# Kernel tuning notes

Measured on AMD Instinct MI355X. Metric: run time of the kernel, lower is better.

The kernel has to match this reference:

```python
import jax, jax.numpy as jnp
import numpy as np

BN_EPS = 1e-5

def relu6(v):
    return jnp.clip(v, 0.0, 6.0)

def setup_inputs() -> dict:
    key = jax.random.key(0)
    ks = jax.random.split(key, 7)
    C, R = 512, 128  # in_channels, reduced_channels = C // 4
    B, H, W = 8, 128, 128
    x = jax.random.normal(ks[0], (B, C, H, W), dtype=jnp.float32)
    # 1x1 convs stored as [out_ch, in_ch] matrices (kernel is 1x1, no bias)
    w_guide = jax.random.normal(ks[1], (R, C), dtype=jnp.float32) * (1.0 / np.sqrt(C))
    w_fuse = jax.random.normal(ks[2], (C, R), dtype=jnp.float32) * (1.0 / np.sqrt(R))
    bn_gamma = jax.random.normal(ks[3], (C,), dtype=jnp.float32) * 0.1 + 1.0
    bn_beta = jax.random.normal(ks[4], (C,), dtype=jnp.float32) * 0.1
    bn_mean = jax.random.normal(ks[5], (C,), dtype=jnp.float32) * 0.1
    bn_var = jax.random.uniform(ks[6], (C,), dtype=jnp.float32, minval=0.5, maxval=1.5)
    return {"x": x, "w_guide": w_guide, "w_fuse": w_fuse,
            "bn_gamma": bn_gamma, "bn_beta": bn_beta,
            "bn_mean": bn_mean, "bn_var": bn_var}

def reference(x, w_guide, w_fuse, bn_gamma, bn_beta, bn_mean, bn_var):
    # y = AdaptiveAvgPool2d(1)(x): [B, C]
    y = jnp.mean(x, axis=(2, 3))
    # conv_guide: 1x1 conv (no bias) + ReLU6 on the 1x1 map -> [B, R]
    y = relu6(jnp.einsum('rc,bc->br', w_guide, y))
    # Nearest upsample of a 1x1 map then pointwise conv+BN+ReLU6 commutes:
    # compute conv_fuse once per (b, channel), then broadcast over H, W.
    y = jnp.einsum('cr,br->bc', w_fuse, y)  # 1x1 conv, no bias -> [B, C]
    inv_std = jax.lax.rsqrt(bn_var + BN_EPS)
    y = relu6((y - bn_mean) * inv_std * bn_gamma + bn_beta)
    # residual add with nearest-broadcast of the constant spatial map
    return x + y[:, :, None, None]
```

## Files before the change

kernel.cpp:

```cpp
#include <hip/hip_runtime.h>

#define C_CH  512
#define R_CH  128
#define BATCH 8
#define HW    16384
#define HW4   (HW / 4)
#define NPLANE (BATCH * C_CH)
#define PPB   4
#define NBLK  (NPLANE / PPB)

typedef float floatx4 __attribute__((ext_vector_type(4)));

__device__ __forceinline__ float relu6f(float v) {
    return fminf(fmaxf(v, 0.0f), 6.0f);
}

__global__ __launch_bounds__(256) void mean_kernel(const float4* __restrict__ x,
                                                   float* __restrict__ meanv) {
    const int plane = blockIdx.x;
    const float4* px = x + (size_t)plane * HW4;
    float s = 0.0f;
#pragma unroll
    for (int it = 0; it < HW4 / 256; ++it) {
        float4 v = px[threadIdx.x + it * 256];
        s += (v.x + v.y) + (v.z + v.w);
    }
    __shared__ float red[256];
    red[threadIdx.x] = s;
    __syncthreads();
    for (int off = 128; off > 0; off >>= 1) {
        if (threadIdx.x < off) red[threadIdx.x] += red[threadIdx.x + off];
        __syncthreads();
    }
    if (threadIdx.x == 0) meanv[plane] = red[0] * (1.0f / (float)HW);
}

__global__ __launch_bounds__(256) void fused_kernel(
    const float4* __restrict__ x,
    const float* __restrict__ meanv,
    const float* __restrict__ wg,
    const float* __restrict__ wf,
    const float* __restrict__ gamma,
    const float* __restrict__ beta,
    const float* __restrict__ mu,
    const float* __restrict__ var,
    float4* __restrict__ out) {
    const int g = (NBLK - 1) - (int)blockIdx.x;
    const int plane0 = g * PPB;
    const int b = plane0 >> 9;
    const int c0 = plane0 & (C_CH - 1);

    __shared__ float m[C_CH];
    __shared__ float part[256];
    __shared__ float t[R_CH];
    __shared__ float yv[PPB];

    const int tid = threadIdx.x;
    for (int c = tid; c < C_CH; c += 256) m[c] = meanv[b * C_CH + c];
    __syncthreads();

    {
        const int r = tid & (R_CH - 1);
        const int half = tid >> 7;
        const float4* w4 = (const float4*)(wg + (size_t)r * C_CH) + half * (C_CH / 8);
        const float* mh = m + half * (C_CH / 2);
        float a0 = 0.f, a1 = 0.f;
#pragma unroll 8
        for (int i = 0; i < C_CH / 8; ++i) {
            float4 v = w4[i];
            const int c = i * 4;
            a0 += v.x * mh[c + 0] + v.y * mh[c + 1];
            a1 += v.z * mh[c + 2] + v.w * mh[c + 3];
        }
        part[tid] = a0 + a1;
    }
    __syncthreads();
    if (tid < R_CH) t[tid] = relu6f(part[tid] + part[tid + R_CH]);
    __syncthreads();

    if (tid < PPB) {
        const int c = c0 + tid;
        const float4* w4 = (const float4*)(wf + (size_t)c * R_CH);
        float a0 = 0.f, a1 = 0.f;
#pragma unroll
        for (int i = 0; i < R_CH / 4; ++i) {
            float4 v = w4[i];
            const int r = i * 4;
            a0 += v.x * t[r + 0] + v.y * t[r + 1];
            a1 += v.z * t[r + 2] + v.w * t[r + 3];
        }
        const float s = a0 + a1;
        const float inv_std = 1.0f / sqrtf(var[c] + 1e-5f);
        yv[tid] = relu6f((s - mu[c]) * inv_std * gamma[c] + beta[c]);
    }
    __syncthreads();

#pragma unroll
    for (int p = 0; p < PPB; ++p) {
        const float a = yv[p];
        const float4* px = x + (size_t)(plane0 + p) * HW4;
        floatx4* po = reinterpret_cast<floatx4*>(out + (size_t)(plane0 + p) * HW4);
#pragma unroll
        for (int it = 0; it < HW4 / 256; ++it) {
            const int i = tid + it * 256;
            float4 v = px[i];
            floatx4 w;
            w.x = v.x + a; w.y = v.y + a; w.z = v.z + a; w.w = v.w + a;
            __builtin_nontemporal_store(w, po + i);
        }
    }
}

extern "C" void kernel_launch(void* const* d_in, const int* in_sizes, int n_in,
                              void* d_out, int out_size, void* d_ws, size_t ws_size,
                              hipStream_t stream) {
    const float4* x4  = (const float4*)d_in[0];
    const float* wg   = (const float*)d_in[1];
    const float* wf   = (const float*)d_in[2];
    const float* gamma = (const float*)d_in[3];
    const float* beta  = (const float*)d_in[4];
    const float* mu    = (const float*)d_in[5];
    const float* var   = (const float*)d_in[6];

    float* meanv = (float*)d_ws;
    float4* out  = (float4*)d_out;

    mean_kernel<<<NPLANE, 256, 0, stream>>>(x4, meanv);
    fused_kernel<<<NBLK, 256, 0, stream>>>(x4, meanv, wg, wf, gamma, beta,
                                           mu, var, out);
}
```

Before: 509.1 us.

## Chunk mean and add passes so second read of x hits cache

Splits the two full passes over x into four chunks of 1024 planes (two batches each). The launches are interleaved: mean for chunk k+1 runs before add for chunk k. The aim is for the second read of each chunk to come from the large last-level cache instead of HBM. It also cuts planes per add block from 4 to 2 and uses nontemporal loads in the add pass. The cost is more kernel launches with smaller grids, plus some risk that the interleaved working set does not stay resident in cache.

Result: slower. 546.1 us (+7.3%).

```diff
diff --git a/kernel.cpp b/kernel.cpp
--- a/kernel.cpp
+++ b/kernel.cpp
@@ -6,8 +6,11 @@
 #define HW    16384
 #define HW4   (HW / 4)
 #define NPLANE (BATCH * C_CH)
-#define PPB   4
-#define NBLK  (NPLANE / PPB)
+#define TPB   256
+#define PPB   2
+#define CHUNK_PLANES 1024
+#define MEAN_BLOCKS  CHUNK_PLANES
+#define ADD_BLOCKS   (CHUNK_PLANES / PPB)
 
 typedef float floatx4 __attribute__((ext_vector_type(4)));
 
@@ -15,28 +18,29 @@
     return fminf(fmaxf(v, 0.0f), 6.0f);
 }
 
-__global__ __launch_bounds__(256) void mean_kernel(const float4* __restrict__ x,
-                                                   float* __restrict__ meanv) {
-    const int plane = blockIdx.x;
+__global__ __launch_bounds__(TPB) void mean_kernel(const float4* __restrict__ x,
+                                                   float* __restrict__ meanv,
+                                                   int plane_base) {
+    const int plane = plane_base + blockIdx.x;
     const float4* px = x + (size_t)plane * HW4;
     float s = 0.0f;
 #pragma unroll
-    for (int it = 0; it < HW4 / 256; ++it) {
-        float4 v = px[threadIdx.x + it * 256];
+    for (int it = 0; it < HW4 / TPB; ++it) {
+        float4 v = px[threadIdx.x + it * TPB];
         s += (v.x + v.y) + (v.z + v.w);
     }
-    __shared__ float red[256];
+    __shared__ float red[TPB];
     red[threadIdx.x] = s;
     __syncthreads();
-    for (int off = 128; off > 0; off >>= 1) {
+    for (int off = TPB / 2; off > 0; off >>= 1) {
         if (threadIdx.x < off) red[threadIdx.x] += red[threadIdx.x + off];
         __syncthreads();
     }
     if (threadIdx.x == 0) meanv[plane] = red[0] * (1.0f / (float)HW);
 }
 
-__global__ __launch_bounds__(256) void fused_kernel(
-    const float4* __restrict__ x,
+__global__ __launch_bounds__(TPB) void add_kernel(
+    const floatx4* __restrict__ x,
     const float* __restrict__ meanv,
     const float* __restrict__ wg,
     const float* __restrict__ wf,
@@ -44,19 +48,19 @@
     const float* __restrict__ beta,
     const float* __restrict__ mu,
     const float* __restrict__ var,
-    float4* __restrict__ out) {
-    const int g = (NBLK - 1) - (int)blockIdx.x;
-    const int plane0 = g * PPB;
-    const int b = plane0 >> 9;
+    floatx4* __restrict__ out,
+    int plane_base) {
+    const int plane0 = plane_base + (int)blockIdx.x * PPB;
+    const int b  = plane0 >> 9;
     const int c0 = plane0 & (C_CH - 1);
+    const int tid = threadIdx.x;
 
     __shared__ float m[C_CH];
-    __shared__ float part[256];
+    __shared__ float part[TPB];
     __shared__ float t[R_CH];
-    __shared__ float yv[PPB];
+    __shared__ float ys[PPB];
 
-    const int tid = threadIdx.x;
-    for (int c = tid; c < C_CH; c += 256) m[c] = meanv[b * C_CH + c];
+    for (int c = tid; c < C_CH; c += TPB) m[c] = meanv[b * C_CH + c];
     __syncthreads();
 
     {
@@ -91,22 +95,21 @@
         }
         const float s = a0 + a1;
         const float inv_std = 1.0f / sqrtf(var[c] + 1e-5f);
-        yv[tid] = relu6f((s - mu[c]) * inv_std * gamma[c] + beta[c]);
+        ys[tid] = relu6f((s - mu[c]) * inv_std * gamma[c] + beta[c]);
     }
     __syncthreads();
 
 #pragma unroll
     for (int p = 0; p < PPB; ++p) {
-        const float a = yv[p];
-        const float4* px = x + (size_t)(plane0 + p) * HW4;
-        floatx4* po = reinterpret_cast<floatx4*>(out + (size_t)(plane0 + p) * HW4);
+        const float a = ys[p];
+        const floatx4* px = x + (size_t)(plane0 + p) * HW4;
+        floatx4* po = out + (size_t)(plane0 + p) * HW4;
 #pragma unroll
-        for (int it = 0; it < HW4 / 256; ++it) {
-            const int i = tid + it * 256;
-            float4 v = px[i];
-            floatx4 w;
-            w.x = v.x + a; w.y = v.y + a; w.z = v.z + a; w.w = v.w + a;
-            __builtin_nontemporal_store(w, po + i);
+        for (int it = 0; it < HW4 / TPB; ++it) {
+            const int i = tid + it * TPB;
+            floatx4 v = __builtin_nontemporal_load(px + i);
+            v += a;
+            __builtin_nontemporal_store(v, po + i);
         }
     }
 }
@@ -114,18 +117,28 @@
 extern "C" void kernel_launch(void* const* d_in, const int* in_sizes, int n_in,
                               void* d_out, int out_size, void* d_ws, size_t ws_size,
                               hipStream_t stream) {
-    const float4* x4  = (const float4*)d_in[0];
-    const float* wg   = (const float*)d_in[1];
-    const float* wf   = (const float*)d_in[2];
-    const float* gamma = (const float*)d_in[3];
-    const float* beta  = (const float*)d_in[4];
-    const float* mu    = (const float*)d_in[5];
-    const float* var   = (const float*)d_in[6];
+    const float4* x4    = (const float4*)d_in[0];
+    const floatx4* xn   = (const floatx4*)d_in[0];
+    const float* wg     = (const float*)d_in[1];
+    const float* wf     = (const float*)d_in[2];
+    const float* gamma  = (const float*)d_in[3];
+    const float* beta   = (const float*)d_in[4];
+    const float* mu     = (const float*)d_in[5];
+    const float* var    = (const float*)d_in[6];
 
-    float* meanv = (float*)d_ws;
-    float4* out  = (float4*)d_out;
+    float* meanv  = (float*)d_ws;
+    floatx4* out  = (floatx4*)d_out;
 
-    mean_kernel<<<NPLANE, 256, 0, stream>>>(x4, meanv);
-    fused_kernel<<<NBLK, 256, 0, stream>>>(x4, meanv, wg, wf, gamma, beta,
-                                           mu, var, out);
+    mean_kernel<<<MEAN_BLOCKS, TPB, 0, stream>>>(x4, meanv, 0 * CHUNK_PLANES);
+    mean_kernel<<<MEAN_BLOCKS, TPB, 0, stream>>>(x4, meanv, 1 * CHUNK_PLANES);
+    add_kernel<<<ADD_BLOCKS, TPB, 0, stream>>>(xn, meanv, wg, wf, gamma, beta,
+                                               mu, var, out, 0 * CHUNK_PLANES);
+    mean_kernel<<<MEAN_BLOCKS, TPB, 0, stream>>>(x4, meanv, 2 * CHUNK_PLANES);
+    add_kernel<<<ADD_BLOCKS, TPB, 0, stream>>>(xn, meanv, wg, wf, gamma, beta,
+                                               mu, var, out, 1 * CHUNK_PLANES);
+    mean_kernel<<<MEAN_BLOCKS, TPB, 0, stream>>>(x4, meanv, 3 * CHUNK_PLANES);
+    add_kernel<<<ADD_BLOCKS, TPB, 0, stream>>>(xn, meanv, wg, wf, gamma, beta,
+                                               mu, var, out, 2 * CHUNK_PLANES);
+    add_kernel<<<ADD_BLOCKS, TPB, 0, stream>>>(xn, meanv, wg, wf, gamma, beta,
+                                               mu, var, out, 3 * CHUNK_PLANES);
 }
```
